# Kernel optimization log

Hardware: AMD Instinct MI355X
Metric: run time of the kernel (lower is better)

Reference implementation:

```python
import jax, jax.numpy as jnp
import numpy as np

EPS = 1e-5
D_MODEL = 64
D_STATE = 16
D_INNER = 128  # expand=2
DT_RANK = 4    # ceil(64/16)


def _inorm(x):
    # InstanceNorm2d (affine=False), NCHW, biased variance, eps=1e-5
    mu = jnp.mean(x, axis=(2, 3), keepdims=True)
    var = jnp.var(x, axis=(2, 3), keepdims=True)
    return (x - mu) * jax.lax.rsqrt(var + EPS)


def _conv2d(x, w, b=None, groups=1):
    y = jax.lax.conv_general_dilated(x, w, (1, 1), 'SAME',
        dimension_numbers=('NCHW', 'OIHW', 'NCHW'), feature_group_count=groups)
    return y if b is None else y + b[None, :, None, None]


def _layernorm(x, w, b):
    mu = jnp.mean(x, axis=-1, keepdims=True)
    var = jnp.var(x, axis=-1, keepdims=True)
    return (x - mu) * jax.lax.rsqrt(var + EPS) * w + b


def _selective_scan(u, delta, A, Bm, Cm, Dp, delta_bias):
    # u, delta: (B,d,L); A: (d,N); Bm,Cm: (B,N,L); Dp: (d,)
    delta = jax.nn.softplus(delta + delta_bias[None, :, None])
    dA = jnp.exp(jnp.einsum('bdl,dn->lbdn', delta, A))        # (L,B,d,N)
    dBu = jnp.einsum('bdl,bnl->lbdn', delta * u, Bm)          # (L,B,d,N)
    Cl = jnp.transpose(Cm, (2, 0, 1))                         # (L,B,N)
    h0 = jnp.zeros((u.shape[0], u.shape[1], A.shape[1]), u.dtype)

    def step(h, inp):
        dA_l, dBu_l, c = inp
        h = dA_l * h + dBu_l
        return h, jnp.einsum('bdn,bn->bd', h, c)

    _, ys = jax.lax.scan(step, h0, (dA, dBu, Cl))             # ys: (L,B,d)
    return jnp.transpose(ys, (1, 2, 0)) + u * Dp[None, :, None]


def _forward(x, dw3_w, dw3_b, dw5_w, dw5_b, dw7_w, dw7_b, fuse_w, fuse_b,
             in_proj_w, conv2d_w, conv2d_b, x_proj_w, dt_proj_w, dt_proj_b,
             A_log, Dp, out_norm_w, out_norm_b, out_proj_w, cf_w, cf_b):
    C = x.shape[1]
    lrelu = lambda t: jax.nn.leaky_relu(t, 0.01)
    # ---- LRGS: multi-scale depthwise convs + fuse + residual (shortcut=Identity) ----
    feats = [lrelu(_inorm(_conv2d(x, w, b, groups=C)))
             for w, b in ((dw3_w, dw3_b), (dw5_w, dw5_b), (dw7_w, dw7_b))]
    xf = _conv2d(jnp.concatenate(feats, axis=1), fuse_w, fuse_b)
    x1 = lrelu(_inorm(xf)) + x
    # ---- MC_Mamba / SS2D ----
    xh = jnp.transpose(x1, (0, 2, 3, 1))           # (B,H,W,C)
    Bn, H, W, _ = xh.shape
    xz = xh @ in_proj_w.T                          # (B,H,W,2*d_inner)
    xm, z = jnp.split(xz, 2, axis=-1)
    xm = jnp.transpose(xm, (0, 3, 1, 2))           # (B,d_inner,H,W)
    xm = jax.nn.silu(_conv2d(xm, conv2d_w, conv2d_b, groups=D_INNER))
    L = H * W
    x_flat = jnp.transpose(xm.reshape(Bn, D_INNER, L), (0, 2, 1))  # (B,L,d)
    xp = x_flat @ x_proj_w.T
    dt, Bm, Cm = jnp.split(xp, [DT_RANK, DT_RANK + D_STATE], axis=-1)
    # NOTE: faithful to source, nn.Linear applies dt_proj_b here AND it is
    # passed again as delta_bias to the scan (bias applied twice).
    dt = jnp.transpose(dt @ dt_proj_w.T + dt_proj_b, (0, 2, 1))    # (B,d,L)
    A = -jnp.exp(A_log)
    y = _selective_scan(jnp.transpose(x_flat, (0, 2, 1)), dt, A,
                        jnp.transpose(Bm, (0, 2, 1)), jnp.transpose(Cm, (0, 2, 1)),
                        Dp, dt_proj_b)
    y = jnp.transpose(y, (0, 2, 1)).reshape(Bn, H, W, D_INNER)
    y = _layernorm(y, out_norm_w, out_norm_b) * jax.nn.silu(z)
    y = y @ out_proj_w.T                           # (B,H,W,d_model)
    y = jnp.transpose(y, (0, 3, 1, 2))
    y = _inorm(_conv2d(y, cf_w, cf_b))
    return x1 + y


def setup_inputs() -> dict:
    key = jax.random.key(0)
    ks = jax.random.split(key, 12)
    B, C, H, W = 8, D_MODEL, 64, 64
    s = 0.05
    return {
        'x': jax.random.normal(ks[0], (B, C, H, W), jnp.float32),
        'dw3_w': jax.random.normal(ks[1], (C, 1, 3, 3), jnp.float32) * s,
        'dw3_b': jnp.zeros((C,), jnp.float32),
        'dw5_w': jax.random.normal(ks[2], (C, 1, 5, 5), jnp.float32) * s,
        'dw5_b': jnp.zeros((C,), jnp.float32),
        'dw7_w': jax.random.normal(ks[3], (C, 1, 7, 7), jnp.float32) * s,
        'dw7_b': jnp.zeros((C,), jnp.float32),
        'fuse_w': jax.random.normal(ks[4], (C, 3 * C, 1, 1), jnp.float32) * s,
        'fuse_b': jnp.zeros((C,), jnp.float32),
        'in_proj_w': jax.random.normal(ks[5], (2 * D_INNER, D_MODEL), jnp.float32) * s,
        'conv2d_w': jax.random.normal(ks[6], (D_INNER, 1, 3, 3), jnp.float32) * s,
        'conv2d_b': jnp.zeros((D_INNER,), jnp.float32),
        'x_proj_w': jax.random.normal(ks[7], (DT_RANK + 2 * D_STATE, D_INNER), jnp.float32) * s,
        'dt_proj_w': jax.random.uniform(ks[8], (D_INNER, DT_RANK), jnp.float32, -0.5, 0.5),
        'dt_proj_b': jnp.exp(jax.random.uniform(ks[9], (D_INNER,), jnp.float32)
                             * (np.log(0.1) - np.log(0.001)) + np.log(0.001)).astype(jnp.float32),
        'A_log': jnp.log(jnp.tile(jnp.arange(1, D_STATE + 1, dtype=jnp.float32), (D_INNER, 1))),
        'Dp': jnp.ones((D_INNER,), jnp.float32),
        'out_norm_w': jnp.ones((D_INNER,), jnp.float32),
        'out_norm_b': jnp.zeros((D_INNER,), jnp.float32),
        'out_proj_w': jax.random.normal(ks[10], (D_MODEL, D_INNER), jnp.float32) * s,
        'cf_w': jax.random.normal(ks[11], (D_MODEL, D_MODEL, 1, 1), jnp.float32) * s,
        'cf_b': jnp.zeros((D_MODEL,), jnp.float32),
    }


def reference(x, dw3_w, dw3_b, dw5_w, dw5_b, dw7_w, dw7_b, fuse_w, fuse_b,
              in_proj_w, conv2d_w, conv2d_b, x_proj_w, dt_proj_w, dt_proj_b,
              A_log, Dp, out_norm_w, out_norm_b, out_proj_w, cf_w, cf_b):
    return _forward(x, dw3_w, dw3_b, dw5_w, dw5_b, dw7_w, dw7_b, fuse_w, fuse_b,
                    in_proj_w, conv2d_w, conv2d_b, x_proj_w, dt_proj_w, dt_proj_b,
                    A_log, Dp, out_norm_w, out_norm_b, out_proj_w, cf_w, cf_b)
```

## Files before the change

### kernel.cpp

```cpp
#include <hip/hip_runtime.h>
#include <math.h>

#define NB 8
#define NC 64
#define NL 4096
#define NDI 128
#define NN 16
#define CHUNK 32
#define NKCH 128

#define OFF_FEATS 0ull
#define OFF_AC    0ull
#define OFF_BC    2097152ull
#define OFF_HINIT 4194304ull
#define OFF_XF    6291456ull
#define OFF_BMAT  6291456ull
#define OFF_CMAT  6815744ull
#define OFF_X1    8388608ull
#define OFF_XMRAW 10485760ull
#define OFF_G     10485760ull
#define OFF_Z     14680064ull
#define OFF_YC    14680064ull
#define OFF_PART  16777216ull
#define OFF_XMC   18874368ull
#define OFF_DTM   23068672ull
#define OFF_WF    27262976ull
#define OFF_WCOMB (OFF_WF + 58624ull)
#define WS_NEED_FLOATS (OFF_WF + 66816ull)

#define WF_DW3    0
#define WF_DW5    576
#define WF_DW7    2176
#define WF_B3     5312
#define WF_B5     5376
#define WF_B7     5440
#define WF_FUSE   5504
#define WF_FUSEB  17792
#define WF_C2W    17856
#define WF_C2B    19008
#define WF_XPW    19136
#define WF_DTW    23744
#define WF_DTB    24256
#define WF_A      24384
#define WF_DP     26432
#define WF_ONW    26560
#define WF_ONB    26688
#define WF_OPW    26816
#define WF_CFW    35008
#define WF_CFB    39104
#define WF_INPJ   39168

struct Cvt { const float* src; float* dst; int n; int op; };
struct CvtArgs { Cvt d[22]; int ncvt; const float* cfw; const float* opw; float* wcomb; };

__global__ __launch_bounds__(256) void k0_cvt(CvtArgs a){
  if ((int)blockIdx.x < a.ncvt){
    Cvt c = a.d[blockIdx.x];
    for (int i = threadIdx.x; i < c.n; i += 256){
      float v = c.src[i];
      c.dst[i] = c.op ? -expf(v) : v;
    }
  } else {
    int idx = (blockIdx.x - a.ncvt)*256 + threadIdx.x;
    int c = idx >> 7, kk = idx & 127;
    float s = 0.f;
    #pragma unroll
    for (int j=0;j<64;j++) s += a.cfw[c*64+j] * a.opw[j*128+kk];
    a.wcomb[idx] = s;
  }
}

__global__ __launch_bounds__(256, 4) void k1_dw(const float* __restrict__ x, const float* __restrict__ wf,
                                                float* __restrict__ feats, float* __restrict__ part){
  const int quar = blockIdx.x & 3, c = (blockIdx.x >> 2) & 63, b = blockIdx.x >> 8;
  const int tid = threadIdx.x;
  const int r0 = quar*16;
  __shared__ float xs[22*73];
  __shared__ float red[4][6];
  for (int i = tid; i < 22*73; i += 256) xs[i] = 0.f;
  const float* xp = x + ((size_t)b*64 + c)*NL;
  float v[6];
  #pragma unroll
  for (int k=0;k<6;k++){
    int idx = tid + k*256;
    int j = idx >> 6, w = idx & 63;
    int gr = r0 - 3 + j;
    bool ok = (idx < 1408) && (gr >= 0) && (gr < 64);
    v[k] = ok ? xp[gr*64 + w] : 0.f;
  }
  float w3r[9], w5r[25], w7r[49];
  #pragma unroll
  for (int i=0;i<9;i++)  w3r[i] = wf[WF_DW3 + c*9 + i];
  #pragma unroll
  for (int i=0;i<25;i++) w5r[i] = wf[WF_DW5 + c*25 + i];
  #pragma unroll
  for (int i=0;i<49;i++) w7r[i] = wf[WF_DW7 + c*49 + i];
  float b3 = wf[WF_B3+c], b5 = wf[WF_B5+c], b7 = wf[WF_B7+c];
  __syncthreads();
  #pragma unroll
  for (int k=0;k<6;k++){
    int idx = tid + k*256;
    if (idx < 1408){
      int j = idx >> 6, w = idx & 63;
      xs[j*73 + (w+3)] = v[k];
    }
  }
  __syncthreads();
  float s3=0,q3=0,s5=0,q5=0,s7=0,q7=0;
  float* f3 = feats + ((size_t)b*192 + c) * NL + r0*64;
  float* f5 = f3 + (size_t)64*NL;
  float* f7 = f3 + (size_t)128*NL;
  {
    int p = tid*4;
    int lh = p >> 6, w0 = p & 63;
    float a3[4], a5[4], a7[4];
    #pragma unroll
    for (int i=0;i<4;i++){ a3[i]=b3; a5[i]=b5; a7[i]=b7; }
    #pragma unroll
    for (int dy=0; dy<7; dy++){
      float s[10];
      #pragma unroll
      for (int j=0;j<10;j++) s[j] = xs[(lh+dy)*73 + w0 + j];
      #pragma unroll
      for (int dx=0;dx<7;dx++){
        float wv = w7r[dy*7+dx];
        #pragma unroll
        for (int i=0;i<4;i++) a7[i] += s[dx+i]*wv;
      }
      if (dy>=1 && dy<=5){
        #pragma unroll
        for (int dx=0;dx<5;dx++){
          float wv = w5r[(dy-1)*5+dx];
          #pragma unroll
          for (int i=0;i<4;i++) a5[i] += s[dx+1+i]*wv;
        }
      }
      if (dy>=2 && dy<=4){
        #pragma unroll
        for (int dx=0;dx<3;dx++){
          float wv = w3r[(dy-2)*3+dx];
          #pragma unroll
          for (int i=0;i<4;i++) a3[i] += s[dx+2+i]*wv;
        }
      }
    }
    *(float4*)(f3+p) = make_float4(a3[0],a3[1],a3[2],a3[3]);
    *(float4*)(f5+p) = make_float4(a5[0],a5[1],a5[2],a5[3]);
    *(float4*)(f7+p) = make_float4(a7[0],a7[1],a7[2],a7[3]);
    #pragma unroll
    for (int i=0;i<4;i++){
      s3+=a3[i]; q3+=a3[i]*a3[i];
      s5+=a5[i]; q5+=a5[i]*a5[i];
      s7+=a7[i]; q7+=a7[i]*a7[i];
    }
  }
  int wid = tid>>6, lane = tid&63;
  float v6[6]={s3,q3,s5,q5,s7,q7};
  #pragma unroll
  for (int j=0;j<6;j++){
    float t = v6[j];
    #pragma unroll
    for (int o=32;o>0;o>>=1) t += __shfl_down(t,o);
    if (!lane) red[wid][j]=t;
  }
  __syncthreads();
  if (tid < 3){
    float su = red[0][tid*2]+red[1][tid*2]+red[2][tid*2]+red[3][tid*2];
    float sq = red[0][tid*2+1]+red[1][tid*2+1]+red[2][tid*2+1]+red[3][tid*2+1];
    size_t k = (size_t)(b*192 + tid*64 + c)*8 + quar*2;
    part[k]   = su;
    part[k+1] = sq;
  }
}

__global__ __launch_bounds__(256, 3) void k2_fuse(const float* __restrict__ feats, const float* __restrict__ npart,
                                                  const float* __restrict__ wf, float* __restrict__ xf){
  int og = blockIdx.x >> 8, rem = blockIdx.x & 255;
  int b = rem >> 5, pt = rem & 31;
  int jslot = threadIdx.x >> 5, pxslot = threadIdx.x & 31;
  __shared__ float wlds2[192][44];
  __shared__ float xs[32][128];
  __shared__ float msl[192], rsl[192];
  for (int i = threadIdx.x; i < 192; i += 256){
    const float* pp = npart + (size_t)(b*192+i)*8;
    float su = pp[0]+pp[2]+pp[4]+pp[6], sq = pp[1]+pp[3]+pp[5]+pp[7];
    float m = su*(1.f/NL);
    msl[i] = m;
    rsl[i] = rsqrtf(sq*(1.f/NL) - m*m + 1e-5f);
  }
  {
    const float* Wg = wf + WF_FUSE + og*32*192;
    for (int i = threadIdx.x; i < 6144; i += 256){
      int o = i / 192, k = i % 192;
      wlds2[k][o] = Wg[i];
    }
  }
  float acc[4][4];
  #pragma unroll
  for (int j=0;j<4;j++)
    #pragma unroll
    for (int p=0;p<4;p++) acc[j][p]=0.f;
  const float* fbase = feats + (size_t)b*192*NL + pt*128;
  for (int ch = 0; ch < 6; ch++){
    __syncthreads();
    for (int i = threadIdx.x; i < 1024; i += 256){
      int r = i >> 5, c4 = i & 31;
      int k = ch*32 + r;
      float4 f = *(const float4*)(fbase + (size_t)k*NL + c4*4);
      float m = msl[k], rs = rsl[k];
      float v0=(f.x-m)*rs, v1=(f.y-m)*rs, v2=(f.z-m)*rs, v3=(f.w-m)*rs;
      v0 = v0>0.f?v0:0.01f*v0; v1 = v1>0.f?v1:0.01f*v1;
      v2 = v2>0.f?v2:0.01f*v2; v3 = v3>0.f?v3:0.01f*v3;
      ((float4*)&xs[r][0])[c4] = make_float4(v0,v1,v2,v3);
    }
    __syncthreads();
    #pragma unroll 1
    for (int c = 0; c < 32; c++){
      float a[4];
      #pragma unroll
      for (int p=0;p<4;p++) a[p] = xs[c][pxslot + 32*p];
      float4 w4 = *(const float4*)&wlds2[ch*32+c][jslot*4];
      float wv[4] = {w4.x, w4.y, w4.z, w4.w};
      #pragma unroll
      for (int jj=0;jj<4;jj++)
        #pragma unroll
        for (int p=0;p<4;p++) acc[jj][p] += wv[jj]*a[p];
    }
  }
  #pragma unroll
  for (int jj=0;jj<4;jj++){
    int o = og*32 + jslot*4 + jj;
    float bias = wf[WF_FUSEB + o];
    float* dp = xf + (size_t)b*64*NL + (size_t)o*NL + pt*128;
    #pragma unroll
    for (int p=0;p<4;p++) dp[pxslot + 32*p] = acc[jj][p] + bias;
  }
}

__global__ __launch_bounds__(256) void k3_norm(const float* __restrict__ xf, const float* __restrict__ x,
                                               float* __restrict__ x1){
  const int tid = threadIdx.x;
  const size_t base = (size_t)blockIdx.x * NL;
  float loc[16]; float s=0.f, q=0.f;
  #pragma unroll
  for (int i=0;i<16;i++){ float v = xf[base + tid + i*256]; loc[i]=v; s+=v; q+=v*v; }
  __shared__ float red[4][2];
  int wid = tid>>6, lane = tid&63;
  #pragma unroll
  for (int o=32;o>0;o>>=1){ s += __shfl_down(s,o); q += __shfl_down(q,o); }
  if (!lane){ red[wid][0]=s; red[wid][1]=q; }
  __syncthreads();
  s = red[0][0]+red[1][0]+red[2][0]+red[3][0];
  q = red[0][1]+red[1][1]+red[2][1]+red[3][1];
  float m = s*(1.f/NL), va = q*(1.f/NL)-m*m, rs = rsqrtf(va+1e-5f);
  #pragma unroll
  for (int i=0;i<16;i++){
    int idx = tid + i*256;
    float v = (loc[i]-m)*rs;
    v = v>0.f ? v : 0.01f*v;
    x1[base+idx] = v + x[base+idx];
  }
}

__global__ __launch_bounds__(256, 4) void k4_inproj(const float* __restrict__ x1, const float* __restrict__ wf,
                                                    float* __restrict__ xmraw, float* __restrict__ z){
  int og = blockIdx.x >> 8, rem = blockIdx.x & 255;
  int b = rem >> 5, pt = rem & 31;
  int jslot = threadIdx.x >> 5, pxslot = threadIdx.x & 31;
  __shared__ float wlds2[64][76];
  __shared__ float xs[32][128];
  {
    const float* Wg = wf + WF_INPJ + og*64*64;
    for (int i = threadIdx.x; i < 4096; i += 256){
      int o = i >> 6, k = i & 63;
      wlds2[k][o] = Wg[i];
    }
  }
  float acc[8][4];
  #pragma unroll
  for (int j=0;j<8;j++)
    #pragma unroll
    for (int p=0;p<4;p++) acc[j][p]=0.f;
  const float* xbase = x1 + (size_t)b*64*NL + pt*128;
  for (int ch = 0; ch < 2; ch++){
    __syncthreads();
    for (int i = threadIdx.x; i < 1024; i += 256){
      int r = i >> 5, c4 = i & 31;
      ((float4*)&xs[r][0])[c4] = *(const float4*)(xbase + (size_t)(ch*32+r)*NL + c4*4);
    }
    __syncthreads();
    #pragma unroll 1
    for (int c = 0; c < 32; c++){
      float a[4];
      #pragma unroll
      for (int p=0;p<4;p++) a[p] = xs[c][pxslot + 32*p];
      const float4* wp = (const float4*)&wlds2[ch*32+c][jslot*8];
      float4 w0 = wp[0], w1 = wp[1];
      float wv[8] = {w0.x,w0.y,w0.z,w0.w, w1.x,w1.y,w1.z,w1.w};
      #pragma unroll
      for (int jj=0;jj<8;jj++)
        #pragma unroll
        for (int p=0;p<4;p++) acc[jj][p] += wv[jj]*a[p];
    }
  }
  float* dstbase = (og < 2 ? xmraw + (size_t)b*128*NL + (size_t)(og*64)*NL
                           : z     + (size_t)b*128*NL + (size_t)((og-2)*64)*NL) + pt*128;
  #pragma unroll
  for (int jj=0;jj<8;jj++){
    float* dp = dstbase + (size_t)(jslot*8+jj)*NL;
    #pragma unroll
    for (int p=0;p<4;p++) dp[pxslot + 32*p] = acc[jj][p];
  }
}

__global__ __launch_bounds__(256, 4) void k5_dw3(const float* __restrict__ xmraw, const float* __restrict__ wf,
                                                 float* __restrict__ xmc){
  const int half = blockIdx.x & 1;
  const int d = (blockIdx.x >> 1) & 127;
  const int bd = blockIdx.x >> 1;
  const int tid = threadIdx.x;
  const int r0 = half*32;
  __shared__ float xs[34*69];
  for (int i=tid;i<34*69;i+=256) xs[i]=0.f;
  const float* xp = xmraw + (size_t)bd * NL;
  float v[9];
  #pragma unroll
  for (int k=0;k<9;k++){
    int idx = tid + k*256;
    int j = idx >> 6, w = idx & 63;
    int gr = r0 - 1 + j;
    bool ok = (idx < 2176) && (gr >= 0) && (gr < 64);
    v[k] = ok ? xp[gr*64 + w] : 0.f;
  }
  float wr[9];
  #pragma unroll
  for (int i=0;i<9;i++) wr[i] = wf[WF_C2W + d*9 + i];
  float bb = wf[WF_C2B + d];
  __syncthreads();
  #pragma unroll
  for (int k=0;k<9;k++){
    int idx = tid + k*256;
    if (idx < 2176){
      int j = idx >> 6, w = idx & 63;
      xs[j*69 + (w+1)] = v[k];
    }
  }
  __syncthreads();
  float* op = xmc + (size_t)bd * NL + r0*64;
  #pragma unroll
  for (int g=0; g<2; g++){
    int p = g*1024 + tid*4;
    int lh = p>>6, w0 = p&63;
    float a[4];
    #pragma unroll
    for (int i=0;i<4;i++) a[i]=bb;
    #pragma unroll
    for (int dy=0; dy<3; dy++){
      float s[6];
      #pragma unroll
      for (int j=0;j<6;j++) s[j] = xs[(lh+dy)*69 + w0 + j];
      #pragma unroll
      for (int dx=0;dx<3;dx++){
        float wv = wr[dy*3+dx];
        #pragma unroll
        for (int i=0;i<4;i++) a[i] += s[dx+i]*wv;
      }
    }
    float4 o;
    o.x = a[0]/(1.f+__expf(-a[0]));
    o.y = a[1]/(1.f+__expf(-a[1]));
    o.z = a[2]/(1.f+__expf(-a[2]));
    o.w = a[3]/(1.f+__expf(-a[3]));
    *(float4*)(op+p) = o;
  }
}

__global__ __launch_bounds__(256, 3) void k6_xproj(const float* __restrict__ xmc, const float* __restrict__ wf,
                                                   float* __restrict__ Bm, float* __restrict__ Cm,
                                                   float* __restrict__ dtm){
  int b = blockIdx.x >> 5, pt = blockIdx.x & 31;
  int jslot = threadIdx.x >> 6, pxslot = threadIdx.x & 63;
  __shared__ float wlds2[128][52];
  __shared__ float xs[32][128];
  {
    const float* Wg = wf + WF_XPW;
    for (int i = threadIdx.x; i < 4608; i += 256){
      int o = i >> 7, k = i & 127;
      wlds2[k][(o/9)*12 + (o%9)] = Wg[i];
    }
  }
  float acc[9][2];
  #pragma unroll
  for (int j=0;j<9;j++){ acc[j][0]=0.f; acc[j][1]=0.f; }
  const float* ubase = xmc + (size_t)b*128*NL + pt*128;
  for (int ch = 0; ch < 4; ch++){
    __syncthreads();
    for (int i = threadIdx.x; i < 1024; i += 256){
      int r = i >> 5, c4 = i & 31;
      ((float4*)&xs[r][0])[c4] = *(const float4*)(ubase + (size_t)(ch*32+r)*NL + c4*4);
    }
    __syncthreads();
    #pragma unroll 1
    for (int c = 0; c < 32; c++){
      float a0 = xs[c][pxslot];
      float a1 = xs[c][pxslot + 64];
      const float* wr = &wlds2[ch*32+c][jslot*12];
      float4 wa = *(const float4*)wr;
      float4 wb = *(const float4*)(wr+4);
      float w8 = wr[8];
      float wv[9] = {wa.x,wa.y,wa.z,wa.w, wb.x,wb.y,wb.z,wb.w, w8};
      #pragma unroll
      for (int j=0;j<9;j++){
        acc[j][0] += wv[j]*a0;
        acc[j][1] += wv[j]*a1;
      }
    }
  }
  #pragma unroll
  for (int j=0;j<9;j++){
    int o = jslot*9 + j;
    float* dp;
    if (o < 4)       dp = dtm + ((size_t)b*4 + o)*NL;
    else if (o < 20) dp = Bm  + ((size_t)b*16 + (o-4))*NL;
    else             dp = Cm  + ((size_t)b*16 + (o-20))*NL;
    dp[pt*128 + pxslot]      = acc[j][0];
    dp[pt*128 + pxslot + 64] = acc[j][1];
  }
}

__global__ __launch_bounds__(128, 2) void k7_scan1(const float* __restrict__ xmc, const float* __restrict__ Bm,
                                                   const float* __restrict__ dtm, const float* __restrict__ wf,
                                                   float* __restrict__ Ac, float* __restrict__ Bc){
  int k = blockIdx.x & (NKCH-1), b = blockIdx.x >> 7;
  int d = threadIdx.x;
  int l0 = k*CHUNK;
  __shared__ float xs[128*33];
  __shared__ float Bl2[32*20];
  __shared__ float dtl2[32*4];
  float vx[32], vb[4], vd;
  #pragma unroll
  for (int j=0;j<32;j++){
    int i = d + 128*j;
    int ch = i >> 5, px = i & 31;
    vx[j] = xmc[((size_t)b*128+ch)*NL + l0 + px];
  }
  #pragma unroll
  for (int j=0;j<4;j++){
    int i = d + 128*j;
    int n = i >> 5, li = i & 31;
    vb[j] = Bm[((size_t)b*16+n)*NL + l0 + li];
  }
  { int n = d >> 5, li = d & 31; vd = dtm[((size_t)b*4+n)*NL + l0 + li]; }
  #pragma unroll
  for (int j=0;j<32;j++){
    int i = d + 128*j;
    int ch = i >> 5, px = i & 31;
    xs[ch*33+px] = vx[j];
  }
  #pragma unroll
  for (int j=0;j<4;j++){
    int i = d + 128*j;
    int n = i >> 5, li = i & 31;
    Bl2[li*20+n] = vb[j];
  }
  { int n = d >> 5, li = d & 31; dtl2[li*4+n] = vd; }
  float A[16], P[16], Q[16];
  const float* Af = wf + WF_A + d*16;
  #pragma unroll
  for (int n=0;n<16;n++){ A[n]=Af[n]; P[n]=1.f; Q[n]=0.f; }
  float w0 = wf[WF_DTW+d*4], w1 = wf[WF_DTW+d*4+1], w2 = wf[WF_DTW+d*4+2], w3 = wf[WF_DTW+d*4+3];
  float db2 = 2.f*wf[WF_DTB+d];
  __syncthreads();
  for (int l=0; l<CHUNK; l++){
    float4 dt4 = ((const float4*)dtl2)[l];
    float tt = w0*dt4.x + w1*dt4.y + w2*dt4.z + w3*dt4.w + db2;
    float de = tt > 20.f ? tt : __logf(1.f+__expf(tt));
    float du = de * xs[d*33+l];
    const float4* bp = (const float4*)(Bl2 + l*20);
    float4 b0 = bp[0], b1 = bp[1], b2 = bp[2], b3 = bp[3];
    float bb[16] = {b0.x,b0.y,b0.z,b0.w, b1.x,b1.y,b1.z,b1.w,
                    b2.x,b2.y,b2.z,b2.w, b3.x,b3.y,b3.z,b3.w};
    #pragma unroll
    for (int n=0;n<16;n++){
      float a = __expf(de*A[n]);
      P[n] *= a;
      Q[n] = a*Q[n] + du*bb[n];
    }
  }
  size_t base = (((size_t)k*NB + b)*128 + d)*16;
  #pragma unroll
  for (int i=0;i<4;i++){
    ((float4*)(Ac+base))[i] = make_float4(P[i*4],P[i*4+1],P[i*4+2],P[i*4+3]);
    ((float4*)(Bc+base))[i] = make_float4(Q[i*4],Q[i*4+1],Q[i*4+2],Q[i*4+3]);
  }
}

__global__ __launch_bounds__(128, 2) void k8_mid(const float* __restrict__ Ac, const float* __restrict__ Bc,
                                                 float* __restrict__ Hi){
  int idx = blockIdx.x*128 + threadIdx.x;
  float h = 0.f;
  for (int k0=0;k0<NKCH;k0+=16){
    float av[16], bv[16];
    #pragma unroll
    for (int j=0;j<16;j++){
      size_t o = (size_t)(k0+j)*16384 + idx;
      av[j]=Ac[o]; bv[j]=Bc[o];
    }
    #pragma unroll
    for (int j=0;j<16;j++){
      size_t o = (size_t)(k0+j)*16384 + idx;
      Hi[o] = h;
      h = av[j]*h + bv[j];
    }
  }
}

__global__ __launch_bounds__(128, 2) void k9_scan2(const float* __restrict__ xmc, const float* __restrict__ Bm,
                                                   const float* __restrict__ Cm, const float* __restrict__ dtm,
                                                   const float* __restrict__ z, const float* __restrict__ wf,
                                                   const float* __restrict__ Hi, float* __restrict__ G){
  int k = blockIdx.x & (NKCH-1), b = blockIdx.x >> 7;
  int d = threadIdx.x;
  int l0 = k*CHUNK;
  __shared__ float xs[128*33];
  __shared__ float Bl2[32*20], Cl2[32*20];
  __shared__ float dtl2[32*4];
  __shared__ float red[4][32][2];
  __shared__ float mstat[32], rstat[32];
  float vx[32], vb[4], vc[4], vd;
  #pragma unroll
  for (int j=0;j<32;j++){
    int i = d + 128*j;
    int ch = i >> 5, px = i & 31;
    vx[j] = xmc[((size_t)b*128+ch)*NL + l0 + px];
  }
  #pragma unroll
  for (int j=0;j<4;j++){
    int i = d + 128*j;
    int n = i >> 5, li = i & 31;
    vb[j] = Bm[((size_t)b*16+n)*NL + l0 + li];
    vc[j] = Cm[((size_t)b*16+n)*NL + l0 + li];
  }
  { int n = d >> 5, li = d & 31; vd = dtm[((size_t)b*4+n)*NL + l0 + li]; }
  float A[16], h[16];
  const float* Af = wf + WF_A + d*16;
  size_t hb = (((size_t)k*NB + b)*128 + d)*16;
  #pragma unroll
  for (int n=0;n<16;n++){ A[n]=Af[n]; h[n]=Hi[hb+n]; }
  #pragma unroll
  for (int j=0;j<32;j++){
    int i = d + 128*j;
    int ch = i >> 5, px = i & 31;
    xs[ch*33+px] = vx[j];
  }
  #pragma unroll
  for (int j=0;j<4;j++){
    int i = d + 128*j;
    int n = i >> 5, li = i & 31;
    Bl2[li*20+n] = vb[j];
    Cl2[li*20+n] = vc[j];
  }
  { int n = d >> 5, li = d & 31; dtl2[li*4+n] = vd; }
  float Dv = wf[WF_DP + d];
  float w0 = wf[WF_DTW+d*4], w1 = wf[WF_DTW+d*4+1], w2 = wf[WF_DTW+d*4+2], w3 = wf[WF_DTW+d*4+3];
  float db2 = 2.f*wf[WF_DTB+d];
  __syncthreads();
  for (int l=0; l<CHUNK; l++){
    float4 dt4 = ((const float4*)dtl2)[l];
    float tt = w0*dt4.x + w1*dt4.y + w2*dt4.z + w3*dt4.w + db2;
    float de = tt > 20.f ? tt : __logf(1.f+__expf(tt));
    float uu = xs[d*33+l];
    float du = de * uu;
    float yv = uu * Dv;
    const float4* bp = (const float4*)(Bl2 + l*20);
    const float4* cp = (const float4*)(Cl2 + l*20);
    float4 b0 = bp[0], b1 = bp[1], b2 = bp[2], b3 = bp[3];
    float4 c0 = cp[0], c1 = cp[1], c2 = cp[2], c3 = cp[3];
    float bb[16] = {b0.x,b0.y,b0.z,b0.w, b1.x,b1.y,b1.z,b1.w,
                    b2.x,b2.y,b2.z,b2.w, b3.x,b3.y,b3.z,b3.w};
    float cc[16] = {c0.x,c0.y,c0.z,c0.w, c1.x,c1.y,c1.z,c1.w,
                    c2.x,c2.y,c2.z,c2.w, c3.x,c3.y,c3.z,c3.w};
    #pragma unroll
    for (int n=0;n<16;n++){
      float a = __expf(de*A[n]);
      h[n] = a*h[n] + du*bb[n];
      yv  += h[n]*cc[n];
    }
    xs[d*33+l] = yv;
  }
  __syncthreads();
  {
    int px = d & 31, q = d >> 5;
    float s=0.f, qq=0.f;
    #pragma unroll
    for (int j=0;j<32;j++){ float v = xs[(q*32+j)*33+px]; s+=v; qq+=v*v; }
    red[q][px][0]=s; red[q][px][1]=qq;
  }
  __syncthreads();
  if (d < 32){
    float ss = red[0][d][0]+red[1][d][0]+red[2][d][0]+red[3][d][0];
    float sq = red[0][d][1]+red[1][d][1]+red[2][d][1]+red[3][d][1];
    float m = ss*(1.f/128.f);
    mstat[d] = m;
    rstat[d] = rsqrtf(sq*(1.f/128.f) - m*m + 1e-5f);
  }
  __syncthreads();
  float ow = wf[WF_ONW+d], ob = wf[WF_ONB+d];
  const float* zp = z + ((size_t)b*128+d)*NL + l0;
  float* gp = G + ((size_t)b*128+d)*NL + l0;
  #pragma unroll
  for (int l4=0; l4<CHUNK/4; l4++){
    float4 zv4 = ((const float4*)zp)[l4];
    float zv[4] = {zv4.x, zv4.y, zv4.z, zv4.w};
    float out[4];
    #pragma unroll
    for (int j=0;j<4;j++){
      int l = l4*4+j;
      float t = (xs[d*33+l]-mstat[l])*rstat[l]*ow + ob;
      out[j] = t * (zv[j]/(1.f+__expf(-zv[j])));
    }
    ((float4*)gp)[l4] = make_float4(out[0],out[1],out[2],out[3]);
  }
}

__global__ __launch_bounds__(256, 4) void k11A_proj(const float* __restrict__ G, const float* __restrict__ wf,
                                                    const float* __restrict__ wcomb,
                                                    float* __restrict__ yc, float* __restrict__ part){
  int og = blockIdx.x >> 8, rem = blockIdx.x & 255;
  int b = rem >> 5, pt = rem & 31;
  int jslot = threadIdx.x >> 5, pxslot = threadIdx.x & 31;
  __shared__ float wlds2[128][44];
  __shared__ float xs[32][128];
  {
    const float* Wg = wcomb + og*32*128;
    for (int i = threadIdx.x; i < 4096; i += 256){
      int o = i >> 7, k = i & 127;
      wlds2[k][o] = Wg[i];
    }
  }
  float acc[4][4];
  #pragma unroll
  for (int j=0;j<4;j++)
    #pragma unroll
    for (int p=0;p<4;p++) acc[j][p]=0.f;
  const float* gbase = G + (size_t)b*128*NL + pt*128;
  for (int ch = 0; ch < 4; ch++){
    __syncthreads();
    for (int i = threadIdx.x; i < 1024; i += 256){
      int r = i >> 5, c4 = i & 31;
      ((float4*)&xs[r][0])[c4] = *(const float4*)(gbase + (size_t)(ch*32+r)*NL + c4*4);
    }
    __syncthreads();
    #pragma unroll 1
    for (int c = 0; c < 32; c++){
      float a[4];
      #pragma unroll
      for (int p=0;p<4;p++) a[p] = xs[c][pxslot + 32*p];
      float4 w4 = *(const float4*)&wlds2[ch*32+c][jslot*4];
      float wv[4] = {w4.x, w4.y, w4.z, w4.w};
      #pragma unroll
      for (int jj=0;jj<4;jj++)
        #pragma unroll
        for (int p=0;p<4;p++) acc[jj][p] += wv[jj]*a[p];
    }
  }
  #pragma unroll
  for (int jj=0;jj<4;jj++){
    int cc = og*32 + jslot*4 + jj;
    float bias = wf[WF_CFB + cc];
    float* dp = yc + (size_t)b*64*NL + (size_t)cc*NL + pt*128;
    float sv = 0.f, qv = 0.f;
    #pragma unroll
    for (int p=0;p<4;p++){
      float t = acc[jj][p] + bias;
      dp[pxslot + 32*p] = t;
      sv += t; qv += t*t;
    }
    #pragma unroll
    for (int o=16;o>0;o>>=1){ sv += __shfl_xor(sv,o); qv += __shfl_xor(qv,o); }
    if (pxslot == 0){
      size_t pidx = (((size_t)b*64 + cc)*32 + pt)*2;
      part[pidx] = sv; part[pidx+1] = qv;
    }
  }
}

__global__ __launch_bounds__(256) void k11c_final(const float* __restrict__ yc, const float* __restrict__ part,
                                                  const float* __restrict__ x1, float* __restrict__ out){
  int bc = blockIdx.x;
  __shared__ float sm, sr;
  if (threadIdx.x == 0){
    float s=0.f, q=0.f;
    #pragma unroll
    for (int t2=0;t2<32;t2++){ s += part[((size_t)bc*32+t2)*2]; q += part[((size_t)bc*32+t2)*2+1]; }
    float m = s*(1.f/NL);
    sm = m; sr = rsqrtf(q*(1.f/NL) - m*m + 1e-5f);
  }
  __syncthreads();
  float m = sm, rs = sr;
  size_t base = (size_t)bc*NL;
  for (int i=threadIdx.x;i<NL;i+=256){
    float v = (yc[base+i]-m)*rs;
    out[base+i] = x1[base+i] + v;
  }
}

extern "C" void kernel_launch(void* const* d_in, const int* in_sizes, int n_in,
                              void* d_out, int out_size, void* d_ws, size_t ws_size,
                              hipStream_t stream) {
  if (ws_size < WS_NEED_FLOATS * sizeof(float)) return;
  const float* x     = (const float*)d_in[0];
  const float* dw3w  = (const float*)d_in[1];
  const float* dw3b  = (const float*)d_in[2];
  const float* dw5w  = (const float*)d_in[3];
  const float* dw5b  = (const float*)d_in[4];
  const float* dw7w  = (const float*)d_in[5];
  const float* dw7b  = (const float*)d_in[6];
  const float* fusew = (const float*)d_in[7];
  const float* fuseb = (const float*)d_in[8];
  const float* inpjw = (const float*)d_in[9];
  const float* c2w   = (const float*)d_in[10];
  const float* c2b   = (const float*)d_in[11];
  const float* xpw   = (const float*)d_in[12];
  const float* dtw   = (const float*)d_in[13];
  const float* dtb   = (const float*)d_in[14];
  const float* alog  = (const float*)d_in[15];
  const float* dpv   = (const float*)d_in[16];
  const float* onw   = (const float*)d_in[17];
  const float* onb   = (const float*)d_in[18];
  const float* opw   = (const float*)d_in[19];
  const float* cfw   = (const float*)d_in[20];
  const float* cfb   = (const float*)d_in[21];

  float* ws    = (float*)d_ws;
  float* wf    = ws + OFF_WF;
  float* wcomb = ws + OFF_WCOMB;
  float* feats = ws + OFF_FEATS;
  float* xf    = ws + OFF_XF;
  float* x1    = ws + OFF_X1;
  float* xmraw = ws + OFF_XMRAW;
  float* z     = ws + OFF_Z;
  float* xmc   = ws + OFF_XMC;
  float* Bmw   = ws + OFF_BMAT;
  float* Cmw   = ws + OFF_CMAT;
  float* dtm   = ws + OFF_DTM;
  float* Acb   = ws + OFF_AC;
  float* Bcb   = ws + OFF_BC;
  float* Hi    = ws + OFF_HINIT;
  float* G     = ws + OFF_G;
  float* yc    = ws + OFF_YC;
  float* part  = ws + OFF_PART;

  CvtArgs ca; int ns = 0;
  auto add = [&](const float* s, int off, int n, int op){
    ca.d[ns].src = s; ca.d[ns].dst = wf + off; ca.d[ns].n = n; ca.d[ns].op = op; ns++;
  };
  add(dw3w, WF_DW3, 576, 0);   add(dw5w, WF_DW5, 1600, 0);  add(dw7w, WF_DW7, 3136, 0);
  add(dw3b, WF_B3, 64, 0);     add(dw5b, WF_B5, 64, 0);     add(dw7b, WF_B7, 64, 0);
  add(fusew, WF_FUSE, 12288, 0); add(fuseb, WF_FUSEB, 64, 0);
  add(c2w, WF_C2W, 1152, 0);   add(c2b, WF_C2B, 128, 0);
  add(xpw, WF_XPW, 4608, 0);   add(dtw, WF_DTW, 512, 0);    add(dtb, WF_DTB, 128, 0);
  add(alog, WF_A, 2048, 1);
  add(dpv, WF_DP, 128, 0);
  add(onw, WF_ONW, 128, 0);    add(onb, WF_ONB, 128, 0);
  add(opw, WF_OPW, 8192, 0);
  add(cfw, WF_CFW, 4096, 0);   add(cfb, WF_CFB, 64, 0);
  add(inpjw, WF_INPJ, 16384, 0);
  ca.ncvt = ns; ca.cfw = cfw; ca.opw = opw; ca.wcomb = wcomb;

  k0_cvt<<<ns + 32, 256, 0, stream>>>(ca);
  k1_dw<<<2048, 256, 0, stream>>>(x, wf, feats, part);
  k2_fuse<<<512, 256, 0, stream>>>(feats, part, wf, xf);
  k3_norm<<<512, 256, 0, stream>>>(xf, x, x1);
  k4_inproj<<<1024, 256, 0, stream>>>(x1, wf, xmraw, z);
  k5_dw3<<<2048, 256, 0, stream>>>(xmraw, wf, xmc);
  k6_xproj<<<256, 256, 0, stream>>>(xmc, wf, Bmw, Cmw, dtm);
  k7_scan1<<<1024, 128, 0, stream>>>(xmc, Bmw, dtm, wf, Acb, Bcb);
  k8_mid<<<128, 128, 0, stream>>>(Acb, Bcb, Hi);
  k9_scan2<<<1024, 128, 0, stream>>>(xmc, Bmw, Cmw, dtm, z, wf, Hi, G);
  k11A_proj<<<512, 256, 0, stream>>>(G, wf, wcomb, yc, part);
  k11c_final<<<512, 256, 0, stream>>>(yc, part, x1, (float*)d_out);
}
```

Measured before the change: 207.3 us.

## Halve scan chunk length and replace per-state exp with power chain when A is -(n+1)

Cuts the chunked selective-scan chunk length from 32 to 16, which doubles the number of chunks and blocks and raises the occupancy hint to 4 blocks per CU. The mid-scan now writes its initial states in place over the chunk-decay buffer, and the chunk-sum buffer moves to another workspace region. When each A row matches -(1..16), a runtime check switches to a path that computes exp(-delta) once and gets exp(-n*delta) by repeated multiplication, avoiding 16 exps per step. This trades more work in the sequential mid-scan and extra buffer traffic for more parallelism. The repeated products may also lose a little precision.

```diff
diff --git a/kernel.cpp b/kernel.cpp
--- a/kernel.cpp
+++ b/kernel.cpp
@@ -6,18 +6,17 @@
 #define NL 4096
 #define NDI 128
 #define NN 16
-#define CHUNK 32
-#define NKCH 128
+#define CHUNK 16
+#define NKCH 256
 
 #define OFF_FEATS 0ull
 #define OFF_AC    0ull
-#define OFF_BC    2097152ull
-#define OFF_HINIT 4194304ull
 #define OFF_XF    6291456ull
 #define OFF_BMAT  6291456ull
 #define OFF_CMAT  6815744ull
 #define OFF_X1    8388608ull
 #define OFF_XMRAW 10485760ull
+#define OFF_BC    10485760ull
 #define OFF_G     10485760ull
 #define OFF_Z     14680064ull
 #define OFF_YC    14680064ull
@@ -428,46 +427,50 @@
   }
 }
 
-__global__ __launch_bounds__(128, 2) void k7_scan1(const float* __restrict__ xmc, const float* __restrict__ Bm,
+__global__ __launch_bounds__(128, 4) void k7_scan1(const float* __restrict__ xmc, const float* __restrict__ Bm,
                                                    const float* __restrict__ dtm, const float* __restrict__ wf,
                                                    float* __restrict__ Ac, float* __restrict__ Bc){
-  int k = blockIdx.x & (NKCH-1), b = blockIdx.x >> 7;
+  int k = blockIdx.x & (NKCH-1), b = blockIdx.x >> 8;
   int d = threadIdx.x;
   int l0 = k*CHUNK;
-  __shared__ float xs[128*33];
-  __shared__ float Bl2[32*20];
-  __shared__ float dtl2[32*4];
-  float vx[32], vb[4], vd;
-  #pragma unroll
-  for (int j=0;j<32;j++){
+  __shared__ float xs[128*17];
+  __shared__ float Bl2[16*20];
+  __shared__ float dtl2[16*4];
+  float vx[16], vb[2], vd = 0.f;
+  #pragma unroll
+  for (int j=0;j<16;j++){
     int i = d + 128*j;
-    int ch = i >> 5, px = i & 31;
+    int ch = i >> 4, px = i & 15;
     vx[j] = xmc[((size_t)b*128+ch)*NL + l0 + px];
   }
   #pragma unroll
-  for (int j=0;j<4;j++){
+  for (int j=0;j<2;j++){
     int i = d + 128*j;
-    int n = i >> 5, li = i & 31;
+    int n = i >> 4, li = i & 15;
     vb[j] = Bm[((size_t)b*16+n)*NL + l0 + li];
   }
-  { int n = d >> 5, li = d & 31; vd = dtm[((size_t)b*4+n)*NL + l0 + li]; }
-  #pragma unroll
-  for (int j=0;j<32;j++){
+  if (d < 64){ int n = d >> 4, li = d & 15; vd = dtm[((size_t)b*4+n)*NL + l0 + li]; }
+  #pragma unroll
+  for (int j=0;j<16;j++){
     int i = d + 128*j;
-    int ch = i >> 5, px = i & 31;
-    xs[ch*33+px] = vx[j];
-  }
-  #pragma unroll
-  for (int j=0;j<4;j++){
+    int ch = i >> 4, px = i & 15;
+    xs[ch*17+px] = vx[j];
+  }
+  #pragma unroll
+  for (int j=0;j<2;j++){
     int i = d + 128*j;
-    int n = i >> 5, li = i & 31;
+    int n = i >> 4, li = i & 15;
     Bl2[li*20+n] = vb[j];
   }
-  { int n = d >> 5, li = d & 31; dtl2[li*4+n] = vd; }
+  if (d < 64){ int n = d >> 4, li = d & 15; dtl2[li*4+n] = vd; }
   float A[16], P[16], Q[16];
   const float* Af = wf + WF_A + d*16;
-  #pragma unroll
-  for (int n=0;n<16;n++){ A[n]=Af[n]; P[n]=1.f; Q[n]=0.f; }
+  bool fastA = true;
+  #pragma unroll
+  for (int n=0;n<16;n++){
+    A[n]=Af[n]; P[n]=1.f; Q[n]=0.f;
+    fastA = fastA && (fabsf(A[n] + (float)(n+1)) < 1e-3f);
+  }
   float w0 = wf[WF_DTW+d*4], w1 = wf[WF_DTW+d*4+1], w2 = wf[WF_DTW+d*4+2], w3 = wf[WF_DTW+d*4+3];
   float db2 = 2.f*wf[WF_DTB+d];
   __syncthreads();
@@ -475,16 +478,27 @@
     float4 dt4 = ((const float4*)dtl2)[l];
     float tt = w0*dt4.x + w1*dt4.y + w2*dt4.z + w3*dt4.w + db2;
     float de = tt > 20.f ? tt : __logf(1.f+__expf(tt));
-    float du = de * xs[d*33+l];
+    float du = de * xs[d*17+l];
     const float4* bp = (const float4*)(Bl2 + l*20);
     float4 b0 = bp[0], b1 = bp[1], b2 = bp[2], b3 = bp[3];
     float bb[16] = {b0.x,b0.y,b0.z,b0.w, b1.x,b1.y,b1.z,b1.w,
                     b2.x,b2.y,b2.z,b2.w, b3.x,b3.y,b3.z,b3.w};
-    #pragma unroll
-    for (int n=0;n<16;n++){
-      float a = __expf(de*A[n]);
-      P[n] *= a;
-      Q[n] = a*Q[n] + du*bb[n];
+    if (fastA){
+      float r = __expf(-de);
+      float ap = 1.f;
+      #pragma unroll
+      for (int n=0;n<16;n++){
+        ap *= r;
+        P[n] *= ap;
+        Q[n] = ap*Q[n] + du*bb[n];
+      }
+    } else {
+      #pragma unroll
+      for (int n=0;n<16;n++){
+        float a = __expf(de*A[n]);
+        P[n] *= a;
+        Q[n] = a*Q[n] + du*bb[n];
+      }
     }
   }
   size_t base = (((size_t)k*NB + b)*128 + d)*16;
@@ -495,8 +509,8 @@
   }
 }
 
-__global__ __launch_bounds__(128, 2) void k8_mid(const float* __restrict__ Ac, const float* __restrict__ Bc,
-                                                 float* __restrict__ Hi){
+__global__ __launch_bounds__(128, 2) void k8_mid(const float* Ac, const float* __restrict__ Bc,
+                                                 float* Hi){
   int idx = blockIdx.x*128 + threadIdx.x;
   float h = 0.f;
   for (int k0=0;k0<NKCH;k0+=16){
@@ -515,52 +529,56 @@
   }
 }
 
-__global__ __launch_bounds__(128, 2) void k9_scan2(const float* __restrict__ xmc, const float* __restrict__ Bm,
+__global__ __launch_bounds__(128, 4) void k9_scan2(const float* __restrict__ xmc, const float* __restrict__ Bm,
                                                    const float* __restrict__ Cm, const float* __restrict__ dtm,
                                                    const float* __restrict__ z, const float* __restrict__ wf,
                                                    const float* __restrict__ Hi, float* __restrict__ G){
-  int k = blockIdx.x & (NKCH-1), b = blockIdx.x >> 7;
+  int k = blockIdx.x & (NKCH-1), b = blockIdx.x >> 8;
   int d = threadIdx.x;
   int l0 = k*CHUNK;
-  __shared__ float xs[128*33];
-  __shared__ float Bl2[32*20], Cl2[32*20];
-  __shared__ float dtl2[32*4];
-  __shared__ float red[4][32][2];
-  __shared__ float mstat[32], rstat[32];
-  float vx[32], vb[4], vc[4], vd;
-  #pragma unroll
-  for (int j=0;j<32;j++){
+  __shared__ float xs[128*17];
+  __shared__ float Bl2[16*20], Cl2[16*20];
+  __shared__ float dtl2[16*4];
+  __shared__ float red[8][16][2];
+  __shared__ float mstat[16], rstat[16];
+  float vx[16], vb[2], vc[2], vd = 0.f;
+  #pragma unroll
+  for (int j=0;j<16;j++){
     int i = d + 128*j;
-    int ch = i >> 5, px = i & 31;
+    int ch = i >> 4, px = i & 15;
     vx[j] = xmc[((size_t)b*128+ch)*NL + l0 + px];
   }
   #pragma unroll
-  for (int j=0;j<4;j++){
+  for (int j=0;j<2;j++){
     int i = d + 128*j;
-    int n = i >> 5, li = i & 31;
+    int n = i >> 4, li = i & 15;
     vb[j] = Bm[((size_t)b*16+n)*NL + l0 + li];
     vc[j] = Cm[((size_t)b*16+n)*NL + l0 + li];
   }
-  { int n = d >> 5, li = d & 31; vd = dtm[((size_t)b*4+n)*NL + l0 + li]; }
+  if (d < 64){ int n = d >> 4, li = d & 15; vd = dtm[((size_t)b*4+n)*NL + l0 + li]; }
   float A[16], h[16];
   const float* Af = wf + WF_A + d*16;
   size_t hb = (((size_t)k*NB + b)*128 + d)*16;
-  #pragma unroll
-  for (int n=0;n<16;n++){ A[n]=Af[n]; h[n]=Hi[hb+n]; }
-  #pragma unroll
-  for (int j=0;j<32;j++){
+  bool fastA = true;
+  #pragma unroll
+  for (int n=0;n<16;n++){
+    A[n]=Af[n]; h[n]=Hi[hb+n];
+    fastA = fastA && (fabsf(A[n] + (float)(n+1)) < 1e-3f);
+  }
+  #pragma unroll
+  for (int j=0;j<16;j++){
     int i = d + 128*j;
-    int ch = i >> 5, px = i & 31;
-    xs[ch*33+px] = vx[j];
-  }
-  #pragma unroll
-  for (int j=0;j<4;j++){
+    int ch = i >> 4, px = i & 15;
+    xs[ch*17+px] = vx[j];
+  }
+  #pragma unroll
+  for (int j=0;j<2;j++){
     int i = d + 128*j;
-    int n = i >> 5, li = i & 31;
+    int n = i >> 4, li = i & 15;
     Bl2[li*20+n] = vb[j];
     Cl2[li*20+n] = vc[j];
   }
-  { int n = d >> 5, li = d & 31; dtl2[li*4+n] = vd; }
+  if (d < 64){ int n = d >> 4, li = d & 15; dtl2[li*4+n] = vd; }
   float Dv = wf[WF_DP + d];
   float w0 = wf[WF_DTW+d*4], w1 = wf[WF_DTW+d*4+1], w2 = wf[WF_DTW+d*4+2], w3 = wf[WF_DTW+d*4+3];
   float db2 = 2.f*wf[WF_DTB+d];
@@ -569,7 +587,7 @@
     float4 dt4 = ((const float4*)dtl2)[l];
     float tt = w0*dt4.x + w1*dt4.y + w2*dt4.z + w3*dt4.w + db2;
     float de = tt > 20.f ? tt : __logf(1.f+__expf(tt));
-    float uu = xs[d*33+l];
+    float uu = xs[d*17+l];
     float du = de * uu;
     float yv = uu * Dv;
     const float4* bp = (const float4*)(Bl2 + l*20);
@@ -580,26 +598,38 @@
                     b2.x,b2.y,b2.z,b2.w, b3.x,b3.y,b3.z,b3.w};
     float cc[16] = {c0.x,c0.y,c0.z,c0.w, c1.x,c1.y,c1.z,c1.w,
                     c2.x,c2.y,c2.z,c2.w, c3.x,c3.y,c3.z,c3.w};
-    #pragma unroll
-    for (int n=0;n<16;n++){
-      float a = __expf(de*A[n]);
-      h[n] = a*h[n] + du*bb[n];
-      yv  += h[n]*cc[n];
-    }
-    xs[d*33+l] = yv;
+    if (fastA){
+      float r = __expf(-de);
+      float ap = 1.f;
+      #pragma unroll
+      for (int n=0;n<16;n++){
+        ap *= r;
+        h[n] = ap*h[n] + du*bb[n];
+        yv  += h[n]*cc[n];
+      }
+    } else {
+      #pragma unroll
+      for (int n=0;n<16;n++){
+        float a = __expf(de*A[n]);
+        h[n] = a*h[n] + du*bb[n];
+        yv  += h[n]*cc[n];
+      }
+    }
+    xs[d*17+l] = yv;
   }
   __syncthreads();
   {
-    int px = d & 31, q = d >> 5;
+    int px = d & 15, q = d >> 4;
     float s=0.f, qq=0.f;
     #pragma unroll
-    for (int j=0;j<32;j++){ float v = xs[(q*32+j)*33+px]; s+=v; qq+=v*v; }
+    for (int j=0;j<16;j++){ float v = xs[(q*16+j)*17+px]; s+=v; qq+=v*v; }
     red[q][px][0]=s; red[q][px][1]=qq;
   }
   __syncthreads();
-  if (d < 32){
-    float ss = red[0][d][0]+red[1][d][0]+red[2][d][0]+red[3][d][0];
-    float sq = red[0][d][1]+red[1][d][1]+red[2][d][1]+red[3][d][1];
+  if (d < 16){
+    float ss=0.f, sq=0.f;
+    #pragma unroll
+    for (int q=0;q<8;q++){ ss += red[q][d][0]; sq += red[q][d][1]; }
     float m = ss*(1.f/128.f);
     mstat[d] = m;
     rstat[d] = rsqrtf(sq*(1.f/128.f) - m*m + 1e-5f);
@@ -616,7 +646,7 @@
     #pragma unroll
     for (int j=0;j<4;j++){
       int l = l4*4+j;
-      float t = (xs[d*33+l]-mstat[l])*rstat[l]*ow + ob;
+      float t = (xs[d*17+l]-mstat[l])*rstat[l]*ow + ob;
       out[j] = t * (zv[j]/(1.f+__expf(-zv[j])));
     }
     ((float4*)gp)[l4] = make_float4(out[0],out[1],out[2],out[3]);
@@ -746,7 +776,6 @@
   float* dtm   = ws + OFF_DTM;
   float* Acb   = ws + OFF_AC;
   float* Bcb   = ws + OFF_BC;
-  float* Hi    = ws + OFF_HINIT;
   float* G     = ws + OFF_G;
   float* yc    = ws + OFF_YC;
   float* part  = ws + OFF_PART;
@@ -775,9 +804,9 @@
   k4_inproj<<<1024, 256, 0, stream>>>(x1, wf, xmraw, z);
   k5_dw3<<<2048, 256, 0, stream>>>(xmraw, wf, xmc);
   k6_xproj<<<256, 256, 0, stream>>>(xmc, wf, Bmw, Cmw, dtm);
-  k7_scan1<<<1024, 128, 0, stream>>>(xmc, Bmw, dtm, wf, Acb, Bcb);
-  k8_mid<<<128, 128, 0, stream>>>(Acb, Bcb, Hi);
-  k9_scan2<<<1024, 128, 0, stream>>>(xmc, Bmw, Cmw, dtm, z, wf, Hi, G);
+  k7_scan1<<<2048, 128, 0, stream>>>(xmc, Bmw, dtm, wf, Acb, Bcb);
+  k8_mid<<<128, 128, 0, stream>>>(Acb, Bcb, Acb );
+  k9_scan2<<<2048, 128, 0, stream>>>(xmc, Bmw, Cmw, dtm, z, wf, Acb , G);
   k11A_proj<<<512, 256, 0, stream>>>(G, wf, wcomb, yc, part);
   k11c_final<<<512, 256, 0, stream>>>(yc, part, x1, (float*)d_out);
 }
```

After: 207.1 us. Within noise of the previous version (-0.1%).
